# Kernel optimization log

Hardware: AMD Instinct MI355X
Metric: run time of the kernel (lower is better)

Reference implementation:

```python
import jax, jax.numpy as jnp
import numpy as np

B, T, E = 2, 2048, 1024
H = 16            # num_heads (global in source repo)
D = E // H        # head_len
LN_EPS = 1e-5


def setup_inputs() -> dict:
    key = jax.random.key(0)
    ks = jax.random.split(key, 12)
    s = lambda fan_in: 1.0 / np.sqrt(fan_in)
    return {
        "x":     jax.random.normal(ks[0], (B, T, E), jnp.float32),
        "ln1_g": jnp.ones((E,), jnp.float32),
        "ln1_b": jnp.zeros((E,), jnp.float32),
        "Wq":    jax.random.normal(ks[1], (E, E), jnp.float32) * s(E),
        "Wk":    jax.random.normal(ks[2], (E, E), jnp.float32) * s(E),
        "Wv":    jax.random.normal(ks[3], (E, E), jnp.float32) * s(E),
        "Wo":    jax.random.normal(ks[4], (E, E), jnp.float32) * s(E),
        "bo":    jnp.zeros((E,), jnp.float32),
        "ln2_g": jnp.ones((E,), jnp.float32),
        "ln2_b": jnp.zeros((E,), jnp.float32),
        "W1":    jax.random.normal(ks[5], (E, 4 * E), jnp.float32) * s(E),
        "b1":    jnp.zeros((4 * E,), jnp.float32),
        "W2":    jax.random.normal(ks[6], (4 * E, E), jnp.float32) * s(4 * E),
        "b2":    jnp.zeros((E,), jnp.float32),
    }


def _layernorm(x, g, b):
    mu = jnp.mean(x, axis=-1, keepdims=True)
    var = jnp.mean(jnp.square(x - mu), axis=-1, keepdims=True)
    return (x - mu) * jax.lax.rsqrt(var + LN_EPS) * g + b


def _attention(x, Wq, Wk, Wv, Wo, bo):
    b, t, e = x.shape
    q = (x @ Wq).reshape(b, t, H, D)
    k = (x @ Wk).reshape(b, t, H, D)
    v = (x @ Wv).reshape(b, t, H, D)
    scores = jnp.einsum("bqhd,bkhd->bhqk", q, k) / np.sqrt(D).astype(np.float32)
    causal = jnp.tril(jnp.ones((t, t), bool))
    scores = jnp.where(causal, scores, -jnp.inf)
    attn = jax.nn.softmax(scores, axis=-1)
    out = jnp.einsum("bhqk,bkhd->bqhd", attn, v).reshape(b, t, e)
    return out @ Wo + bo


def reference(x, ln1_g, ln1_b, Wq, Wk, Wv, Wo, bo, ln2_g, ln2_b, W1, b1, W2, b2):
    # pre-norm attention + residual (dropout=0 / eval mode)
    x = x + _attention(_layernorm(x, ln1_g, ln1_b), Wq, Wk, Wv, Wo, bo)
    # pre-norm MLP + residual
    h = _layernorm(x, ln2_g, ln2_b)
    h = jax.nn.relu(h @ W1 + b1) @ W2 + b2
    return x + h
```

## Files before the change

### kernel.cpp

```cpp
#include <hip/hip_runtime.h>
#include <cmath>
#include <cstdint>
#include <cstddef>

typedef __bf16 bf16_t;
typedef __bf16 bf16x8 __attribute__((ext_vector_type(8)));
typedef float  f32x4  __attribute__((ext_vector_type(4)));

#define B_   2
#define T_   2048
#define E_   1024
#define H_   16
#define D_   64
#define FF_  4096
#define NROW (B_ * T_)
#define QS_  (3 * E_)
#define NTI  (T_ / 64)

__global__ __launch_bounds__(256) void ln_kernel(
    const float* __restrict__ x, const float* __restrict__ g,
    const float* __restrict__ bta, bf16_t* __restrict__ out)
{
    int row = blockIdx.x;
    int tid = threadIdx.x;
    const float4* xr = (const float4*)(x + (size_t)row * E_);
    float4 v = xr[tid];
    float s  = v.x + v.y + v.z + v.w;
    float ss = v.x * v.x + v.y * v.y + v.z * v.z + v.w * v.w;
#pragma unroll
    for (int off = 32; off; off >>= 1) {
        s  += __shfl_xor(s, off);
        ss += __shfl_xor(ss, off);
    }
    __shared__ float red[8];
    int wave = tid >> 6, lane = tid & 63;
    if (lane == 0) { red[wave] = s; red[4 + wave] = ss; }
    __syncthreads();
    s  = red[0] + red[1] + red[2] + red[3];
    ss = red[4] + red[5] + red[6] + red[7];
    float mu   = s * (1.0f / E_);
    float var  = ss * (1.0f / E_) - mu * mu;
    float rstd = rsqrtf(var + 1e-5f);
    float4 gv = ((const float4*)g)[tid];
    float4 bv = ((const float4*)bta)[tid];
    union { bf16_t h[4]; ushort4 u; } pk;
    pk.h[0] = (bf16_t)((v.x - mu) * rstd * gv.x + bv.x);
    pk.h[1] = (bf16_t)((v.y - mu) * rstd * gv.y + bv.y);
    pk.h[2] = (bf16_t)((v.z - mu) * rstd * gv.z + bv.z);
    pk.h[3] = (bf16_t)((v.w - mu) * rstd * gv.w + bv.w);
    ((ushort4*)(out + (size_t)row * E_))[tid] = pk.u;
}

__global__ __launch_bounds__(256) void ln_reduce2(
    const float* __restrict__ p, const float* __restrict__ bias,
    const float* __restrict__ resid, float* __restrict__ x1,
    const float* __restrict__ g, const float* __restrict__ bta,
    bf16_t* __restrict__ out)
{
    int row = blockIdx.x;
    int tid = threadIdx.x;
    size_t off = (size_t)row * E_;
    float4 v0 = ((const float4*)(p + off))[tid];
    float4 v1 = ((const float4*)(p + (size_t)NROW * E_ + off))[tid];
    float4 bb = ((const float4*)bias)[tid];
    float4 rr = ((const float4*)(resid + off))[tid];
    float4 v;
    v.x = v0.x + v1.x + bb.x + rr.x;
    v.y = v0.y + v1.y + bb.y + rr.y;
    v.z = v0.z + v1.z + bb.z + rr.z;
    v.w = v0.w + v1.w + bb.w + rr.w;
    ((float4*)(x1 + off))[tid] = v;
    float s  = v.x + v.y + v.z + v.w;
    float ss = v.x * v.x + v.y * v.y + v.z * v.z + v.w * v.w;
#pragma unroll
    for (int o = 32; o; o >>= 1) {
        s  += __shfl_xor(s, o);
        ss += __shfl_xor(ss, o);
    }
    __shared__ float red[8];
    int wave = tid >> 6, lane = tid & 63;
    if (lane == 0) { red[wave] = s; red[4 + wave] = ss; }
    __syncthreads();
    s  = red[0] + red[1] + red[2] + red[3];
    ss = red[4] + red[5] + red[6] + red[7];
    float mu   = s * (1.0f / E_);
    float var  = ss * (1.0f / E_) - mu * mu;
    float rstd = rsqrtf(var + 1e-5f);
    float4 gv = ((const float4*)g)[tid];
    float4 bv = ((const float4*)bta)[tid];
    union { bf16_t h[4]; ushort4 u; } pk;
    pk.h[0] = (bf16_t)((v.x - mu) * rstd * gv.x + bv.x);
    pk.h[1] = (bf16_t)((v.y - mu) * rstd * gv.y + bv.y);
    pk.h[2] = (bf16_t)((v.z - mu) * rstd * gv.z + bv.z);
    pk.h[3] = (bf16_t)((v.w - mu) * rstd * gv.w + bv.w);
    ((ushort4*)(out + off))[tid] = pk.u;
}

__global__ __launch_bounds__(256) void add_reduce2(
    const float* __restrict__ p, const float* __restrict__ bias,
    const float* __restrict__ resid, float* __restrict__ out)
{
    int row = blockIdx.x;
    int tid = threadIdx.x;
    size_t off = (size_t)row * E_;
    float4 v0 = ((const float4*)(p + off))[tid];
    float4 v1 = ((const float4*)(p + (size_t)NROW * E_ + off))[tid];
    float4 bb = ((const float4*)bias)[tid];
    float4 rr = ((const float4*)(resid + off))[tid];
    float4 v;
    v.x = v0.x + v1.x + bb.x + rr.x;
    v.y = v0.y + v1.y + bb.y + rr.y;
    v.z = v0.z + v1.z + bb.z + rr.z;
    v.w = v0.w + v1.w + bb.w + rr.w;
    ((float4*)(out + off))[tid] = v;
}

__global__ __launch_bounds__(256) void transpose_all(
    const float* __restrict__ Wq, const float* __restrict__ Wk,
    const float* __restrict__ Wv, const float* __restrict__ Wo,
    const float* __restrict__ W1, const float* __restrict__ W2,
    bf16_t* __restrict__ wqkv, bf16_t* __restrict__ wot,
    bf16_t* __restrict__ w1t, bf16_t* __restrict__ w2t)
{
    int l = blockIdx.x;
    const float* W; bf16_t* Wt; int K, N, bx, by;
    if (l < 4096) {
        int seg = l >> 10, r = l & 1023;
        K = E_; N = E_; bx = r & 31; by = r >> 5;
        if      (seg == 0) { W = Wq; Wt = wqkv; }
        else if (seg == 1) { W = Wk; Wt = wqkv + (size_t)E_ * E_; }
        else if (seg == 2) { W = Wv; Wt = wqkv + (size_t)2 * E_ * E_; }
        else               { W = Wo; Wt = wot; }
    } else if (l < 8192) {
        int r = l - 4096; K = E_; N = FF_; bx = r & 127; by = r >> 7;
        W = W1; Wt = w1t;
    } else {
        int r = l - 8192; K = FF_; N = E_; bx = r & 31; by = r >> 5;
        W = W2; Wt = w2t;
    }
    __shared__ float t[32][33];
    int n0 = bx * 32, k0 = by * 32;
    int tx = threadIdx.x & 31, ty = threadIdx.x >> 5;
#pragma unroll
    for (int i = 0; i < 4; ++i)
        t[ty + i * 8][tx] = W[(size_t)(k0 + ty + i * 8) * N + n0 + tx];
    __syncthreads();
#pragma unroll
    for (int i = 0; i < 4; ++i)
        Wt[(size_t)(n0 + ty + i * 8) * K + k0 + tx] = (bf16_t)t[tx][ty + i * 8];
}

#define BM 128
#define BN 128
#define BK 32

__global__ __launch_bounds__(256) void gemm_bt(
    const bf16_t* __restrict__ A, const bf16_t* __restrict__ Bt,
    const float* __restrict__ bias, const float* __restrict__ resid,
    void* __restrict__ Cout, bf16_t* __restrict__ vt_out,
    int M, int N, int K, int lda, int ldb,
    int has_bias, int do_relu, int has_resid, int out_bf16)
{
    __shared__ __attribute__((aligned(16))) bf16_t As[2][BM * BK];
    __shared__ __attribute__((aligned(16))) bf16_t Bs[2][BN * BK];
    int tid  = threadIdx.x;
    int lane = tid & 63, wave = tid >> 6;
    int m0 = blockIdx.x * BM, n0 = blockIdx.y * BN;
    int wm = (wave & 1) * 64, wn = (wave >> 1) * 64;
    int koff = blockIdx.z * K;
    f32x4 acc[4][4];
#pragma unroll
    for (int i = 0; i < 4; ++i)
#pragma unroll
        for (int j = 0; j < 4; ++j) acc[i][j] = (f32x4){0.f, 0.f, 0.f, 0.f};

    int sr = tid >> 2;
    int sc = (tid & 3) * 8;
    const int kq = (lane >> 4) * 8;
    const int ml = lane & 15;
    const bf16_t* Ag = A  + (size_t)(m0 + sr) * lda + koff + sc;
    const bf16_t* Bg = Bt + (size_t)(n0 + sr) * ldb + koff + sc;
    int niter = K / BK;

    {
        uint4 ra0 = *(const uint4*)Ag;
        uint4 ra1 = *(const uint4*)(Ag + (size_t)64 * lda);
        uint4 rb0 = *(const uint4*)Bg;
        uint4 rb1 = *(const uint4*)(Bg + (size_t)64 * ldb);
        *(uint4*)&As[0][sr * BK + sc]        = ra0;
        *(uint4*)&As[0][(sr + 64) * BK + sc] = ra1;
        *(uint4*)&Bs[0][sr * BK + sc]        = rb0;
        *(uint4*)&Bs[0][(sr + 64) * BK + sc] = rb1;
    }

    for (int it = 0; it < niter; ++it) {
        int cur = it & 1, nxt = cur ^ 1;
        __syncthreads();

        uint4 ra0, ra1, rb0, rb1;
        bool pf = (it + 1 < niter);
        if (pf) {
            int k0 = (it + 1) * BK;
            ra0 = *(const uint4*)(Ag + k0);
            ra1 = *(const uint4*)(Ag + k0 + (size_t)64 * lda);
            rb0 = *(const uint4*)(Bg + k0);
            rb1 = *(const uint4*)(Bg + k0 + (size_t)64 * ldb);
        }

        bf16x8 af[4], bfr[4];
#pragma unroll
        for (int mi = 0; mi < 4; ++mi)
            af[mi] = *(const bf16x8*)&As[cur][(wm + mi * 16 + ml) * BK + kq];
#pragma unroll
        for (int ni = 0; ni < 4; ++ni)
            bfr[ni] = *(const bf16x8*)&Bs[cur][(wn + ni * 16 + ml) * BK + kq];
#pragma unroll
        for (int mi = 0; mi < 4; ++mi)
#pragma unroll
            for (int ni = 0; ni < 4; ++ni)
                acc[mi][ni] = __builtin_amdgcn_mfma_f32_16x16x32_bf16(
                    af[mi], bfr[ni], acc[mi][ni], 0, 0, 0);

        if (pf) {
            *(uint4*)&As[nxt][sr * BK + sc]        = ra0;
            *(uint4*)&As[nxt][(sr + 64) * BK + sc] = ra1;
            *(uint4*)&Bs[nxt][sr * BK + sc]        = rb0;
            *(uint4*)&Bs[nxt][(sr + 64) * BK + sc] = rb1;
        }
    }

    int r4 = (lane >> 4) * 4;
    if (gridDim.z > 1) {
        float* P = (float*)Cout + (size_t)blockIdx.z * M * N;
#pragma unroll
        for (int mi = 0; mi < 4; ++mi)
#pragma unroll
            for (int ni = 0; ni < 4; ++ni) {
                int col = n0 + wn + ni * 16 + ml;
#pragma unroll
                for (int r = 0; r < 4; ++r) {
                    int row = m0 + wm + mi * 16 + r4 + r;
                    P[(size_t)row * N + col] = acc[mi][ni][r];
                }
            }
        return;
    }
    if (vt_out && n0 >= 2 * E_) {
#pragma unroll
        for (int mi = 0; mi < 4; ++mi)
#pragma unroll
            for (int ni = 0; ni < 4; ++ni) {
                int vcol = n0 + wn + ni * 16 + ml - 2 * E_;
                int h = vcol >> 6, d = vcol & 63;
                int row0 = m0 + wm + mi * 16 + r4;
                int b = row0 >> 11, t = row0 & (T_ - 1);
                union { bf16_t h4[4]; uint2 u; } pk;
#pragma unroll
                for (int r = 0; r < 4; ++r) pk.h4[r] = (bf16_t)acc[mi][ni][r];
                *(uint2*)&vt_out[((size_t)(b * H_ + h) * D_ + d) * T_ + t] = pk.u;
            }
        return;
    }
#pragma unroll
    for (int mi = 0; mi < 4; ++mi) {
#pragma unroll
        for (int ni = 0; ni < 4; ++ni) {
            int col = n0 + wn + ni * 16 + ml;
            float bval = has_bias ? bias[col] : 0.0f;
#pragma unroll
            for (int r = 0; r < 4; ++r) {
                int row = m0 + wm + mi * 16 + r4 + r;
                float v = acc[mi][ni][r] + bval;
                if (do_relu)   v = fmaxf(v, 0.0f);
                if (has_resid) v += resid[(size_t)row * N + col];
                if (out_bf16)
                    ((bf16_t*)Cout)[(size_t)row * N + col] = (bf16_t)v;
                else
                    ((float*)Cout)[(size_t)row * N + col] = v;
            }
        }
    }
}

#define PSTR 72

struct TileState {
    f32x4 acc[4];
    float m1, l1;
};

__device__ __forceinline__ void tile_update(
    const bf16x8 kf[2][4], const bf16x8 vf[2][4], const bf16x8 qf[2],
    TileState& st, bf16_t* PsW, int ml, int r4, int kq8,
    bool diag, int ch, int qrow)
{
    f32x4 s[4];
#pragma unroll
    for (int nt = 0; nt < 4; ++nt) {
        s[nt] = (f32x4){0.f, 0.f, 0.f, 0.f};
#pragma unroll
        for (int ks = 0; ks < 2; ++ks)
            s[nt] = __builtin_amdgcn_mfma_f32_16x16x32_bf16(kf[ks][nt], qf[ks], s[nt], 0, 0, 0);
    }
    if (diag) {
#pragma unroll
        for (int nt = 0; nt < 4; ++nt)
#pragma unroll
            for (int r = 0; r < 4; ++r)
                if (ch * 64 + nt * 16 + r4 + r > qrow) s[nt][r] = -INFINITY;
    }
    float mx = -INFINITY;
#pragma unroll
    for (int nt = 0; nt < 4; ++nt)
#pragma unroll
        for (int r = 0; r < 4; ++r) mx = fmaxf(mx, s[nt][r]);
    mx = fmaxf(mx, __shfl_xor(mx, 16));
    mx = fmaxf(mx, __shfl_xor(mx, 32));
    float mn = fmaxf(st.m1, mx);
    float al = __expf(st.m1 - mn);
    st.m1 = mn;
    float sum = 0.f;
#pragma unroll
    for (int nt = 0; nt < 4; ++nt)
#pragma unroll
        for (int r = 0; r < 4; ++r) {
            float p = __expf(s[nt][r] - mn);
            s[nt][r] = p;
            sum += p;
        }
    sum += __shfl_xor(sum, 16);
    sum += __shfl_xor(sum, 32);
    st.l1 = st.l1 * al + sum;
#pragma unroll
    for (int dt = 0; dt < 4; ++dt)
#pragma unroll
        for (int r = 0; r < 4; ++r) st.acc[dt][r] *= al;

#pragma unroll
    for (int nt = 0; nt < 4; ++nt) {
        union { bf16_t h[4]; uint2 u; } pk;
#pragma unroll
        for (int r = 0; r < 4; ++r) pk.h[r] = (bf16_t)s[nt][r];
        *(uint2*)&PsW[ml * PSTR + nt * 16 + r4] = pk.u;
    }
#pragma unroll
    for (int ks = 0; ks < 2; ++ks) {
        bf16x8 pf = *(const bf16x8*)&PsW[ml * PSTR + ks * 32 + kq8];
#pragma unroll
        for (int dt = 0; dt < 4; ++dt)
            st.acc[dt] = __builtin_amdgcn_mfma_f32_16x16x32_bf16(vf[ks][dt], pf, st.acc[dt], 0, 0, 0);
    }
}

__global__ __launch_bounds__(256) void attn_mfma(
    const bf16_t* __restrict__ Qp, const bf16_t* __restrict__ Kp,
    const bf16_t* __restrict__ Vt, bf16_t* __restrict__ O)
{
    __shared__ __attribute__((aligned(16))) bf16_t Ks[2][64 * PSTR];
    __shared__ __attribute__((aligned(16))) bf16_t Vts[2][64 * PSTR];
    __shared__ __attribute__((aligned(16))) bf16_t Ps[4][16 * PSTR];

    int tid = threadIdx.x, lane = tid & 63, wave = tid >> 6;
    int ml  = lane & 15;
    int kq8 = (lane >> 4) * 8;
    int r4  = (lane >> 4) * 4;
    int bh = blockIdx.y, b = bh >> 4, h = bh & 15;
    size_t qk_base = (size_t)b * T_ * QS_ + h * D_;
    size_t vt_base = (size_t)bh * D_ * T_;
    size_t o_base  = (size_t)b * T_ * E_ + h * D_;

    int lo = blockIdx.x, hi = NTI - 1 - blockIdx.x;
    int qlo = lo * 64 + wave * 16;
    int qhi = hi * 64 + wave * 16;

    bf16x8 qfl[2], qfh[2];
#pragma unroll
    for (int ks = 0; ks < 2; ++ks) {
        bf16x8 a = *(const bf16x8*)&Qp[qk_base + (size_t)(qlo + ml) * QS_ + ks * 32 + kq8];
        bf16x8 c = *(const bf16x8*)&Qp[qk_base + (size_t)(qhi + ml) * QS_ + ks * 32 + kq8];
#pragma unroll
        for (int j = 0; j < 8; ++j) {
            a[j] = (bf16_t)((float)a[j] * 0.125f);
            c[j] = (bf16_t)((float)c[j] * 0.125f);
        }
        qfl[ks] = a; qfh[ks] = c;
    }

    TileState stl, sth;
#pragma unroll
    for (int dt = 0; dt < 4; ++dt) {
        stl.acc[dt] = (f32x4){0.f, 0.f, 0.f, 0.f};
        sth.acc[dt] = (f32x4){0.f, 0.f, 0.f, 0.f};
    }
    stl.m1 = -INFINITY; stl.l1 = 0.f;
    sth.m1 = -INFINITY; sth.l1 = 0.f;

    int r0 = tid >> 3, c0 = (tid & 7) * 8;
    int nch = hi + 1;

    {
        const bf16_t* kb = &Kp[qk_base + (size_t)r0 * QS_ + c0];
        const bf16_t* vb = &Vt[vt_base + (size_t)r0 * T_ + c0];
        uint4 k0v = *(const uint4*)kb;
        uint4 k1v = *(const uint4*)(kb + (size_t)32 * QS_);
        uint4 v0v = *(const uint4*)vb;
        uint4 v1v = *(const uint4*)(vb + (size_t)32 * T_);
        *(uint4*)&Ks[0][r0 * PSTR + c0]         = k0v;
        *(uint4*)&Ks[0][(r0 + 32) * PSTR + c0]  = k1v;
        *(uint4*)&Vts[0][r0 * PSTR + c0]        = v0v;
        *(uint4*)&Vts[0][(r0 + 32) * PSTR + c0] = v1v;
    }

    for (int ch = 0; ch < nch; ++ch) {
        int cur = ch & 1, nxt = cur ^ 1;
        __syncthreads();

        uint4 nk0, nk1, nv0, nv1;
        bool pf = (ch + 1 < nch);
        if (pf) {
            const bf16_t* kb = &Kp[qk_base + (size_t)((ch + 1) * 64 + r0) * QS_ + c0];
            const bf16_t* vb = &Vt[vt_base + (size_t)r0 * T_ + (ch + 1) * 64 + c0];
            nk0 = *(const uint4*)kb;
            nk1 = *(const uint4*)(kb + (size_t)32 * QS_);
            nv0 = *(const uint4*)vb;
            nv1 = *(const uint4*)(vb + (size_t)32 * T_);
        }

        bf16x8 kf[2][4], vf[2][4];
#pragma unroll
        for (int ks = 0; ks < 2; ++ks)
#pragma unroll
            for (int nt = 0; nt < 4; ++nt) {
                kf[ks][nt] = *(const bf16x8*)&Ks[cur][(nt * 16 + ml) * PSTR + ks * 32 + kq8];
                vf[ks][nt] = *(const bf16x8*)&Vts[cur][(nt * 16 + ml) * PSTR + ks * 32 + kq8];
            }

        tile_update(kf, vf, qfh, sth, Ps[wave], ml, r4, kq8,
                    ch == hi, ch, qhi + ml);
        if (ch <= lo)
            tile_update(kf, vf, qfl, stl, Ps[wave], ml, r4, kq8,
                        ch == lo, ch, qlo + ml);

        if (pf) {
            *(uint4*)&Ks[nxt][r0 * PSTR + c0]         = nk0;
            *(uint4*)&Ks[nxt][(r0 + 32) * PSTR + c0]  = nk1;
            *(uint4*)&Vts[nxt][r0 * PSTR + c0]        = nv0;
            *(uint4*)&Vts[nxt][(r0 + 32) * PSTR + c0] = nv1;
        }
    }

#pragma unroll
    for (int t = 0; t < 2; ++t) {
        TileState& st = t ? stl : sth;
        int qw = t ? qlo : qhi;
        float inv = 1.0f / st.l1;
#pragma unroll
        for (int dt = 0; dt < 4; ++dt) {
            union { bf16_t h[4]; uint2 u; } pk;
#pragma unroll
            for (int r = 0; r < 4; ++r) pk.h[r] = (bf16_t)(st.acc[dt][r] * inv);
            *(uint2*)&Ps[wave][ml * PSTR + dt * 16 + r4] = pk.u;
        }
        int row = lane >> 2, seg = (lane & 3) * 16;
        bf16x8 o0 = *(const bf16x8*)&Ps[wave][row * PSTR + seg];
        bf16x8 o1 = *(const bf16x8*)&Ps[wave][row * PSTR + seg + 8];
        size_t gp = o_base + (size_t)(qw + row) * E_ + seg;
        *(bf16x8*)&O[gp]     = o0;
        *(bf16x8*)&O[gp + 8] = o1;
    }
}

extern "C" void kernel_launch(void* const* d_in, const int* in_sizes, int n_in,
                              void* d_out, int out_size, void* d_ws, size_t ws_size,
                              hipStream_t stream)
{
    const float* x    = (const float*)d_in[0];
    const float* ln1g = (const float*)d_in[1];
    const float* ln1b = (const float*)d_in[2];
    const float* Wq   = (const float*)d_in[3];
    const float* Wk   = (const float*)d_in[4];
    const float* Wv   = (const float*)d_in[5];
    const float* Wo   = (const float*)d_in[6];
    const float* bo   = (const float*)d_in[7];
    const float* ln2g = (const float*)d_in[8];
    const float* ln2b = (const float*)d_in[9];
    const float* W1   = (const float*)d_in[10];
    const float* b1   = (const float*)d_in[11];
    const float* W2   = (const float*)d_in[12];
    const float* b2   = (const float*)d_in[13];

    char* ws = (char*)d_ws;
    const size_t MB = 1024ull * 1024ull;
    bf16_t* wqkv = (bf16_t*)(ws + 0 * MB);
    bf16_t* wot  = (bf16_t*)(ws + 6 * MB);
    bf16_t* w1t  = (bf16_t*)(ws + 8 * MB);
    bf16_t* w2t  = (bf16_t*)(ws + 16 * MB);
    bf16_t* xn   = (bf16_t*)(ws + 24 * MB);
    bf16_t* QKV  = (bf16_t*)(ws + 32 * MB);
    bf16_t* att  = (bf16_t*)(ws + 56 * MB);
    float*  x1   = (float*)(ws + 64 * MB);
    bf16_t* hb   = (bf16_t*)(ws + 80 * MB);
    bf16_t* h1   = (bf16_t*)(ws + 88 * MB);
    bf16_t* Vtb  = (bf16_t*)(ws + 88 * MB);
    float*  part = (float*)(ws + 24 * MB);

    dim3 blk(256);

    transpose_all<<<dim3(12288), blk, 0, stream>>>(
        Wq, Wk, Wv, Wo, W1, W2, wqkv, wot, w1t, w2t);

    ln_kernel<<<dim3(NROW), blk, 0, stream>>>(x, ln1g, ln1b, xn);

    gemm_bt<<<dim3(NROW / BM, QS_ / BN), blk, 0, stream>>>(
        xn, wqkv, nullptr, nullptr, QKV, Vtb, NROW, QS_, E_, E_, E_, 0, 0, 0, 1);

    attn_mfma<<<dim3(NTI / 2, B_ * H_), blk, 0, stream>>>(
        QKV, QKV + E_, Vtb, att);

    gemm_bt<<<dim3(NROW / BM, E_ / BN, 2), blk, 0, stream>>>(
        att, wot, nullptr, nullptr, part, nullptr, NROW, E_, E_ / 2, E_, E_, 0, 0, 0, 0);
    ln_reduce2<<<dim3(NROW), blk, 0, stream>>>(
        part, bo, x, x1, ln2g, ln2b, hb);

    gemm_bt<<<dim3(NROW / BM, FF_ / BN), blk, 0, stream>>>(
        hb, w1t, b1, nullptr, h1, nullptr, NROW, FF_, E_, E_, E_, 1, 1, 0, 1);

    gemm_bt<<<dim3(NROW / BM, E_ / BN, 2), blk, 0, stream>>>(
        h1, w2t, nullptr, nullptr, part, nullptr, NROW, E_, FF_ / 2, FF_, FF_, 0, 0, 0, 0);
    add_reduce2<<<dim3(NROW), blk, 0, stream>>>(
        part, b2, x1, (float*)d_out);
}
```

Before: 342.1 us.

## Load GEMM tiles directly to LDS with global_load_lds and BK=64

Replaces register-staged double-buffered global-to-LDS copies with direct global_load_lds transfers into a single LDS buffer, and doubles the K tile to 64 so each barrier covers two MFMA k-steps. The aim is to remove the register round-trip and VGPR pressure of staging loads and to halve the number of loop iterations. In exchange, the single buffer means the next tile's loads are issued only after a barrier at the end of compute, so load latency is no longer overlapped with MFMA work within a block and depends on other resident blocks. The LDS layout is unpadded, which risks bank conflicts on the 128-byte row stride.

New measurement: 357.5 us. 4.5% more time.

```diff
diff --git a/kernel.cpp b/kernel.cpp
--- a/kernel.cpp
+++ b/kernel.cpp
@@ -152,7 +152,14 @@
 
 #define BM 128
 #define BN 128
-#define BK 32
+#define BK 64
+
+__device__ __forceinline__ void gload16(const bf16_t* g, bf16_t* l)
+{
+    __builtin_amdgcn_global_load_lds(
+        (const __attribute__((address_space(1))) void*)g,
+        (__attribute__((address_space(3))) void*)l, 16, 0, 0);
+}
 
 __global__ __launch_bounds__(256) void gemm_bt(
     const bf16_t* __restrict__ A, const bf16_t* __restrict__ Bt,
@@ -161,8 +168,8 @@
     int M, int N, int K, int lda, int ldb,
     int has_bias, int do_relu, int has_resid, int out_bf16)
 {
-    __shared__ __attribute__((aligned(16))) bf16_t As[2][BM * BK];
-    __shared__ __attribute__((aligned(16))) bf16_t Bs[2][BN * BK];
+    __shared__ __attribute__((aligned(16))) bf16_t As[BM * BK];
+    __shared__ __attribute__((aligned(16))) bf16_t Bs[BN * BK];
     int tid  = threadIdx.x;
     int lane = tid & 63, wave = tid >> 6;
     int m0 = blockIdx.x * BM, n0 = blockIdx.y * BN;
@@ -174,58 +181,49 @@
 #pragma unroll
         for (int j = 0; j < 4; ++j) acc[i][j] = (f32x4){0.f, 0.f, 0.f, 0.f};
 
-    int sr = tid >> 2;
-    int sc = (tid & 3) * 8;
     const int kq = (lane >> 4) * 8;
     const int ml = lane & 15;
-    const bf16_t* Ag = A  + (size_t)(m0 + sr) * lda + koff + sc;
-    const bf16_t* Bg = Bt + (size_t)(n0 + sr) * ldb + koff + sc;
+
+    int srow = wave * 32 + (lane >> 3);
+    int scol = (lane & 7) * 8;
+    const bf16_t* Ag = A  + (size_t)(m0 + srow) * lda + koff + scol;
+    const bf16_t* Bg = Bt + (size_t)(n0 + srow) * ldb + koff + scol;
+    bf16_t* Asw = &As[wave * 32 * BK];
+    bf16_t* Bsw = &Bs[wave * 32 * BK];
     int niter = K / BK;
 
-    {
-        uint4 ra0 = *(const uint4*)Ag;
-        uint4 ra1 = *(const uint4*)(Ag + (size_t)64 * lda);
-        uint4 rb0 = *(const uint4*)Bg;
-        uint4 rb1 = *(const uint4*)(Bg + (size_t)64 * ldb);
-        *(uint4*)&As[0][sr * BK + sc]        = ra0;
-        *(uint4*)&As[0][(sr + 64) * BK + sc] = ra1;
-        *(uint4*)&Bs[0][sr * BK + sc]        = rb0;
-        *(uint4*)&Bs[0][(sr + 64) * BK + sc] = rb1;
+#pragma unroll
+    for (int j = 0; j < 4; ++j) {
+        gload16(Ag + (size_t)j * 8 * lda, Asw + j * 8 * BK);
+        gload16(Bg + (size_t)j * 8 * ldb, Bsw + j * 8 * BK);
     }
 
     for (int it = 0; it < niter; ++it) {
-        int cur = it & 1, nxt = cur ^ 1;
         __syncthreads();
-
-        uint4 ra0, ra1, rb0, rb1;
-        bool pf = (it + 1 < niter);
-        if (pf) {
+#pragma unroll
+        for (int ks = 0; ks < 2; ++ks) {
+            bf16x8 af[4], bfr[4];
+#pragma unroll
+            for (int mi = 0; mi < 4; ++mi)
+                af[mi] = *(const bf16x8*)&As[(wm + mi * 16 + ml) * BK + ks * 32 + kq];
+#pragma unroll
+            for (int ni = 0; ni < 4; ++ni)
+                bfr[ni] = *(const bf16x8*)&Bs[(wn + ni * 16 + ml) * BK + ks * 32 + kq];
+#pragma unroll
+            for (int mi = 0; mi < 4; ++mi)
+#pragma unroll
+                for (int ni = 0; ni < 4; ++ni)
+                    acc[mi][ni] = __builtin_amdgcn_mfma_f32_16x16x32_bf16(
+                        af[mi], bfr[ni], acc[mi][ni], 0, 0, 0);
+        }
+        if (it + 1 < niter) {
+            __syncthreads();
             int k0 = (it + 1) * BK;
-            ra0 = *(const uint4*)(Ag + k0);
-            ra1 = *(const uint4*)(Ag + k0 + (size_t)64 * lda);
-            rb0 = *(const uint4*)(Bg + k0);
-            rb1 = *(const uint4*)(Bg + k0 + (size_t)64 * ldb);
-        }
-
-        bf16x8 af[4], bfr[4];
-#pragma unroll
-        for (int mi = 0; mi < 4; ++mi)
-            af[mi] = *(const bf16x8*)&As[cur][(wm + mi * 16 + ml) * BK + kq];
-#pragma unroll
-        for (int ni = 0; ni < 4; ++ni)
-            bfr[ni] = *(const bf16x8*)&Bs[cur][(wn + ni * 16 + ml) * BK + kq];
-#pragma unroll
-        for (int mi = 0; mi < 4; ++mi)
-#pragma unroll
-            for (int ni = 0; ni < 4; ++ni)
-                acc[mi][ni] = __builtin_amdgcn_mfma_f32_16x16x32_bf16(
-                    af[mi], bfr[ni], acc[mi][ni], 0, 0, 0);
-
-        if (pf) {
-            *(uint4*)&As[nxt][sr * BK + sc]        = ra0;
-            *(uint4*)&As[nxt][(sr + 64) * BK + sc] = ra1;
-            *(uint4*)&Bs[nxt][sr * BK + sc]        = rb0;
-            *(uint4*)&Bs[nxt][(sr + 64) * BK + sc] = rb1;
+#pragma unroll
+            for (int j = 0; j < 4; ++j) {
+                gload16(Ag + k0 + (size_t)j * 8 * lda, Asw + j * 8 * BK);
+                gload16(Bg + k0 + (size_t)j * 8 * ldb, Bsw + j * 8 * BK);
+            }
         }
     }
 
```
